# Kernel optimization log

Measured on AMD Instinct MI355X. Metric: run time of the kernel, lower is better.

## Reference

```python
import jax, jax.numpy as jnp
import numpy as np

DIM_MODEL = 1024
DIM_K = 1024
DIM_V = 1024


def setup_inputs() -> dict:
    key = jax.random.key(0)
    ks = jax.random.split(key, 7)
    B, S = 4, 2048
    scale = 1.0 / np.sqrt(DIM_MODEL)
    return {
        "x": jax.random.normal(ks[0], (B, S, DIM_MODEL), dtype=jnp.float32),
        # weights stored [in, out] (transpose of torch Linear.weight)
        "Wq": jax.random.normal(ks[1], (DIM_MODEL, DIM_K), dtype=jnp.float32) * scale,
        "Wk": jax.random.normal(ks[2], (DIM_MODEL, DIM_K), dtype=jnp.float32) * scale,
        "Wv": jax.random.normal(ks[3], (DIM_MODEL, DIM_V), dtype=jnp.float32) * scale,
        "Wo": jax.random.normal(ks[4], (DIM_V, DIM_MODEL), dtype=jnp.float32) * (1.0 / np.sqrt(DIM_V)),
        "ln2_gamma": jnp.ones((DIM_MODEL,), dtype=jnp.float32),
        "ln2_beta": jnp.zeros((DIM_MODEL,), dtype=jnp.float32),
    }


def _layernorm(x, gamma, beta, eps=1e-5):
    mu = jnp.mean(x, axis=-1, keepdims=True)
    var = jnp.var(x, axis=-1, keepdims=True)
    return (x - mu) * jax.lax.rsqrt(var + eps) * gamma + beta


def reference(x, Wq, Wk, Wv, Wo, ln2_gamma, ln2_beta):
    # single-head attention, x: [B,S,D]
    q = jnp.einsum("bsd,dk->bsk", x, Wq)
    k = jnp.einsum("bsd,dk->bsk", x, Wk)
    v = jnp.einsum("bsd,dv->bsv", x, Wv)
    scores = jnp.einsum("bqk,bsk->bqs", q, k) / jnp.sqrt(jnp.asarray(DIM_K, x.dtype))
    attn = jax.nn.softmax(scores, axis=-1)  # [B,S,S]
    ctx = jnp.einsum("bqs,bsv->bqv", attn, v)
    hidden = jnp.einsum("bqv,vd->bqd", ctx, Wo)
    hidden = _layernorm(hidden, ln2_gamma, ln2_beta)
    return hidden
```

## Files before the change

### kernel.cpp

```cpp
#include <hip/hip_runtime.h>
#include <hip/hip_bf16.h>
#include <stdint.h>

typedef __bf16 bf16;
typedef __attribute__((ext_vector_type(8))) __bf16 bf16x8;
typedef __attribute__((ext_vector_type(4))) __bf16 bf16x4;
typedef __attribute__((ext_vector_type(4))) float f32x4;

#define AS1 __attribute__((address_space(1)))
#define AS3 __attribute__((address_space(3)))

__device__ __forceinline__ void gl_lds16(const void* g, void* l) {
  __builtin_amdgcn_global_load_lds((const AS1 uint32_t*)g, (AS3 uint32_t*)l, 16, 0, 0);
}

#define FENCE() asm volatile("" ::: "memory")
#define BAR()                        \
  do {                               \
    FENCE();                         \
    __builtin_amdgcn_s_barrier();    \
    FENCE();                         \
  } while (0)
#define VMW4() asm volatile("s_waitcnt vmcnt(4)" ::: "memory")

template <int MODE>
__global__ __launch_bounds__(512, 2) void gemm256(
    const bf16* __restrict__ Abase, const bf16* __restrict__ Bbase,
    bf16* __restrict__ Cbase, int K, int lda, int ldb, int ldc,
    long long sA, long long sB, long long sC, float alpha,
    float* __restrict__ lsum, bf16* __restrict__ C2, bf16* __restrict__ C3) {
  extern __shared__ char smem[];
  const int z = blockIdx.z;
  const bf16* A = Abase + (long long)z * sA;
  const bf16* B = Bbase + (long long)z * sB;
  bf16* C = Cbase + (long long)z * sC;
  const int m0 = blockIdx.y * 256, n0 = blockIdx.x * 256;
  const int t = threadIdx.x;
  const int lane = t & 63;
  const int wid = t >> 6, wrow = wid >> 2, wcol = wid & 3;
  const int quad = lane >> 4, r = lane & 15;

  const int rowq = t >> 3;
  const int chunk = (t & 7) ^ (rowq & 7);
  const bf16* pA0 = A + (long long)(m0 + rowq) * lda + chunk * 8;
  const bf16* pB0 = B + (long long)(n0 + rowq) * ldb + chunk * 8;

  const int aoff = (wrow * 64 + r) * 128;
  const int boff = 32768 + (wcol * 32 + r) * 128;
  const int cs0 = ((quad) ^ (r & 7)) * 16;
  const int cs1 = ((4 + quad) ^ (r & 7)) * 16;

#define STAGE_A(HALF, KT, SB)                                                  \
  do {                                                                         \
    gl_lds16(pA0 + (long long)((HALF) * 128) * lda + (KT),                     \
             (SB) + (HALF) * 16384 + t * 16);                                  \
    gl_lds16(pA0 + (long long)((HALF) * 128 + 64) * lda + (KT),                \
             (SB) + (HALF) * 16384 + 8192 + t * 16);                           \
  } while (0)
#define STAGE_B(HALF, KT, SB)                                                  \
  do {                                                                         \
    gl_lds16(pB0 + (long long)((HALF) * 128) * ldb + (KT),                     \
             (SB) + 32768 + (HALF) * 16384 + t * 16);                          \
    gl_lds16(pB0 + (long long)((HALF) * 128 + 64) * ldb + (KT),                \
             (SB) + 32768 + (HALF) * 16384 + 8192 + t * 16);                   \
  } while (0)
#define READ_A(MH)                                                             \
  _Pragma("unroll") for (int mr = 0; mr < 4; ++mr) {                           \
    af[mr][0] = *(const bf16x8*)(Sc + (MH) * 16384 + aoff + mr * 2048 + cs0);  \
    af[mr][1] = *(const bf16x8*)(Sc + (MH) * 16384 + aoff + mr * 2048 + cs1);  \
  }
#define READ_B(NH)                                                             \
  _Pragma("unroll") for (int nr = 0; nr < 2; ++nr) {                           \
    bfr[NH][nr][0] =                                                           \
        *(const bf16x8*)(Sc + (NH) * 16384 + boff + nr * 2048 + cs0);          \
    bfr[NH][nr][1] =                                                           \
        *(const bf16x8*)(Sc + (NH) * 16384 + boff + nr * 2048 + cs1);          \
  }
#define MMA(MH, NH)                                                            \
  _Pragma("unroll") for (int mr = 0; mr < 4; ++mr)                             \
      _Pragma("unroll") for (int nr = 0; nr < 2; ++nr) {                       \
    acc[MH][NH][mr][nr] = __builtin_amdgcn_mfma_f32_16x16x32_bf16(             \
        af[mr][0], bfr[NH][nr][0], acc[MH][NH][mr][nr], 0, 0, 0);              \
    acc[MH][NH][mr][nr] = __builtin_amdgcn_mfma_f32_16x16x32_bf16(             \
        af[mr][1], bfr[NH][nr][1], acc[MH][NH][mr][nr], 0, 0, 0);              \
  }

  f32x4 acc[2][2][4][2] = {};
  bf16x8 af[4][2];
  bf16x8 bfr[2][2][2];
  char* Sc = smem;
  char* Sn = smem + 65536;
  const int T = K >> 6;

  STAGE_A(0, 0, Sc);
  STAGE_B(0, 0, Sc);
  STAGE_A(1, 0, Sc);
  STAGE_B(1, 0, Sc);
  {
    const int kt1p = (T > 1) ? 64 : 0;
    STAGE_A(0, kt1p, Sn);
    STAGE_B(0, kt1p, Sn);
  }
  VMW4();
  BAR();

  for (int tt = 0; tt < T; ++tt) {
    const int kt1 = (tt + 1 < T ? tt + 1 : 0) << 6;
    const int kt2 = (tt + 2 < T ? tt + 2 : 0) << 6;
    READ_A(0);
    READ_B(0);
    STAGE_A(1, kt1, Sn);
    __builtin_amdgcn_s_setprio(1);
    MMA(0, 0);
    __builtin_amdgcn_s_setprio(0);
    BAR();
    READ_B(1);
    STAGE_B(1, kt1, Sn);
    __builtin_amdgcn_s_setprio(1);
    MMA(0, 1);
    __builtin_amdgcn_s_setprio(0);
    BAR();
    READ_A(1);
    STAGE_A(0, kt2, Sc);
    __builtin_amdgcn_s_setprio(1);
    MMA(1, 0);
    __builtin_amdgcn_s_setprio(0);
    BAR();
    STAGE_B(0, kt2, Sc);
    __builtin_amdgcn_s_setprio(1);
    MMA(1, 1);
    __builtin_amdgcn_s_setprio(0);
    VMW4();
    BAR();
    char* tp = Sc;
    Sc = Sn;
    Sn = tp;
  }

  if constexpr (MODE == 4) {
    bf16* dst;
    int c0;
    if (n0 < 1024) {
      dst = Cbase;
      c0 = n0;
    } else if (n0 < 2048) {
      dst = C2;
      c0 = n0 - 1024;
    } else {
      dst = C3;
      c0 = n0 - 2048;
    }
#pragma unroll
    for (int mh = 0; mh < 2; ++mh)
#pragma unroll
      for (int mr = 0; mr < 4; ++mr) {
        const int row0 = m0 + mh * 128 + wrow * 64 + mr * 16 + quad * 4;
#pragma unroll
        for (int nh = 0; nh < 2; ++nh)
#pragma unroll
          for (int nr = 0; nr < 2; ++nr) {
            const int col = c0 + nh * 128 + wcol * 32 + nr * 16 + r;
#pragma unroll
            for (int rg = 0; rg < 4; ++rg)
              dst[(long long)(row0 + rg) * 1024 + col] =
                  (bf16)acc[mh][nh][mr][nr][rg];
          }
      }
    return;
  }

#pragma unroll
  for (int mh = 0; mh < 2; ++mh)
#pragma unroll
    for (int mr = 0; mr < 4; ++mr) {
      const int row0 = m0 + mh * 128 + wrow * 64 + mr * 16 + quad * 4;
      float rsum[4] = {0.f, 0.f, 0.f, 0.f};
#pragma unroll
      for (int nh = 0; nh < 2; ++nh)
#pragma unroll
        for (int nr = 0; nr < 2; ++nr) {
          const int col = n0 + nh * 128 + wcol * 32 + nr * 16 + r;
#pragma unroll
          for (int rg = 0; rg < 4; ++rg) {
            float v = acc[mh][nh][mr][nr][rg] * alpha;
            if constexpr (MODE == 1) {
              bf16 eb = (bf16)__expf(v);
              C[(long long)(row0 + rg) * ldc + col] = eb;
              rsum[rg] += (float)eb;
            } else {
              C[(long long)(row0 + rg) * ldc + col] = (bf16)v;
            }
          }
        }
      if constexpr (MODE == 1) {
#pragma unroll
        for (int rg = 0; rg < 4; ++rg) {
#pragma unroll
          for (int off = 8; off >= 1; off >>= 1)
            rsum[rg] += __shfl_xor(rsum[rg], off);
          if (r == 0)
            atomicAdd(&lsum[(long long)z * 2048 + row0 + rg], rsum[rg]);
        }
      }
    }
#undef STAGE_A
#undef STAGE_B
#undef READ_A
#undef READ_B
#undef MMA
}

template <int MODE>
__global__ __launch_bounds__(256, 3) void gemm128(
    const bf16* __restrict__ Abase, const bf16* __restrict__ Bbase,
    bf16* __restrict__ Cbase, int K, int lda, int ldb, int ldc,
    long long sA, long long sB, long long sC, float alpha,
    bf16* __restrict__ C2, bf16* __restrict__ C3) {
  extern __shared__ char smem[];
  const int z = blockIdx.z;
  const bf16* A = Abase + (long long)z * sA;
  const bf16* B = Bbase + (long long)z * sB;
  bf16* C = Cbase + (long long)z * sC;
  const int m0 = blockIdx.y * 128, n0 = blockIdx.x * 128;
  const int t = threadIdx.x;
  const int lane = t & 63, wave = t >> 6;
  const int wm = (wave >> 1) * 64, wn = (wave & 1) * 64;
  const int quad = lane >> 4, r = lane & 15;

  const int srow = t >> 3;
  const int schunk = (t & 7) ^ (srow & 7);
  const bf16* ga = A + (long long)(m0 + srow) * lda + schunk * 8;
  const bf16* gb = B + (long long)(n0 + srow) * ldb + schunk * 8;
  char* la = smem + t * 16;
  char* lb = smem + 16384 + t * 16;

  f32x4 acc[4][4] = {};

  for (int k0 = 0; k0 < K; k0 += 64) {
    __syncthreads();
#pragma unroll
    for (int rd = 0; rd < 4; rd++) {
      gl_lds16(ga + (long long)(32 * rd) * lda, la + rd * 4096);
      gl_lds16(gb + (long long)(32 * rd) * ldb, lb + rd * 4096);
    }
    ga += 64;
    gb += 64;
    __syncthreads();

#pragma unroll
    for (int kk = 0; kk < 2; kk++) {
      bf16x8 af[4], bfr[4];
      const int csa = ((kk * 4 + quad) ^ (r & 7)) * 16;
      const char* pa = smem + (wm + r) * 128 + csa;
      const char* pb = smem + 16384 + (wn + r) * 128 + csa;
#pragma unroll
      for (int i = 0; i < 4; i++) af[i] = *(const bf16x8*)(pa + i * 2048);
#pragma unroll
      for (int j = 0; j < 4; j++) bfr[j] = *(const bf16x8*)(pb + j * 2048);
#pragma unroll
      for (int i = 0; i < 4; i++)
#pragma unroll
        for (int j = 0; j < 4; j++)
          acc[i][j] = __builtin_amdgcn_mfma_f32_16x16x32_bf16(af[i], bfr[j],
                                                              acc[i][j], 0, 0, 0);
    }
  }

  if constexpr (MODE == 4) {
    bf16* dst;
    int c0;
    if (n0 < 1024) {
      dst = Cbase; c0 = n0;
    } else if (n0 < 2048) {
      dst = C2; c0 = n0 - 1024;
    } else {
      dst = C3; c0 = n0 - 2048;
    }
#pragma unroll
    for (int i = 0; i < 4; i++) {
      const int row0 = m0 + wm + i * 16 + quad * 4;
#pragma unroll
      for (int j = 0; j < 4; j++) {
        const int col = c0 + wn + j * 16 + r;
#pragma unroll
        for (int rg = 0; rg < 4; rg++)
          dst[(long long)(row0 + rg) * 1024 + col] = (bf16)acc[i][j][rg];
      }
    }
    return;
  }

#pragma unroll
  for (int i = 0; i < 4; i++) {
    const int row0 = m0 + wm + i * 16 + quad * 4;
#pragma unroll
    for (int j = 0; j < 4; j++) {
      const int col = n0 + wn + j * 16 + r;
#pragma unroll
      for (int rg = 0; rg < 4; rg++) {
        float v = acc[i][j][rg] * alpha;
        C[(long long)(row0 + rg) * ldc + col] = (bf16)v;
      }
    }
  }
}

__global__ __launch_bounds__(256) void prep(
    const float* __restrict__ x, const float* __restrict__ Wq,
    const float* __restrict__ Wk, const float* __restrict__ Wv,
    const float* __restrict__ Wo, bf16* __restrict__ Xb,
    bf16* __restrict__ Wcat, bf16* __restrict__ Wot,
    float* __restrict__ lsum) {
  __shared__ float tile[32][33];
  const int bx = blockIdx.x;
  const int t = threadIdx.x;
  if (bx < 4096) {
    if (bx < 32) lsum[bx * 256 + t] = 0.f;
    long long i = (long long)bx * 256 + t;
    const float4* p = (const float4*)x;
    float4 a = p[i * 2], b = p[i * 2 + 1];
    bf16x8 o;
    o[0] = (bf16)a.x; o[1] = (bf16)a.y; o[2] = (bf16)a.z; o[3] = (bf16)a.w;
    o[4] = (bf16)b.x; o[5] = (bf16)b.y; o[6] = (bf16)b.z; o[7] = (bf16)b.w;
    ((bf16x8*)Xb)[i] = o;
  } else {
    int idx = bx - 4096;
    const int zw = idx >> 10;
    idx &= 1023;
    const int tiy = idx >> 5, tix = idx & 31;
    const float* W = (zw == 0) ? Wq : (zw == 1) ? Wk : (zw == 2) ? Wv : Wo;
    bf16* dst = (zw < 3) ? (Wcat + (long long)zw * 1024 * 1024) : Wot;
    const int bx0 = tix * 32, by0 = tiy * 32;
    const int ttx = t & 31, tty = t >> 5;
#pragma unroll
    for (int i = 0; i < 32; i += 8)
      tile[tty + i][ttx] = W[(long long)(by0 + tty + i) * 1024 + bx0 + ttx];
    __syncthreads();
#pragma unroll
    for (int i = 0; i < 32; i += 8)
      dst[(long long)(bx0 + tty + i) * 1024 + by0 + ttx] = (bf16)tile[ttx][tty + i];
  }
}

__global__ __launch_bounds__(256) void layernorm_rows(
    const bf16* __restrict__ H, const float* __restrict__ lsum,
    const float* __restrict__ gamma, const float* __restrict__ beta,
    float* __restrict__ O) {
  const long long row = blockIdx.x;
  const bf16* h = H + row * 1024;
  float* o = O + row * 1024;
  const int t = threadIdx.x;
  const int lane = t & 63, wave = t >> 6;
  const float invl = 1.f / lsum[row];
  bf16x4 hv = ((const bf16x4*)h)[t];
  float v[4] = {(float)hv[0] * invl, (float)hv[1] * invl, (float)hv[2] * invl,
                (float)hv[3] * invl};
  float s = v[0] + v[1] + v[2] + v[3];
  float ss = v[0] * v[0] + v[1] * v[1] + v[2] * v[2] + v[3] * v[3];
#pragma unroll
  for (int off = 32; off >= 1; off >>= 1) {
    s += __shfl_xor(s, off);
    ss += __shfl_xor(ss, off);
  }
  __shared__ float rs[4], rss[4];
  if (lane == 0) {
    rs[wave] = s;
    rss[wave] = ss;
  }
  __syncthreads();
  s = rs[0] + rs[1] + rs[2] + rs[3];
  ss = rss[0] + rss[1] + rss[2] + rss[3];
  const float mean = s * (1.f / 1024.f);
  const float var = ss * (1.f / 1024.f) - mean * mean;
  const float rstd = rsqrtf(var + 1e-5f);
  float4 g = ((const float4*)gamma)[t];
  float4 bb = ((const float4*)beta)[t];
  float4 rr;
  rr.x = (v[0] - mean) * rstd * g.x + bb.x;
  rr.y = (v[1] - mean) * rstd * g.y + bb.y;
  rr.z = (v[2] - mean) * rstd * g.z + bb.z;
  rr.w = (v[3] - mean) * rstd * g.w + bb.w;
  ((float4*)o)[t] = rr;
}

extern "C" void kernel_launch(void* const* d_in, const int* in_sizes, int n_in,
                              void* d_out, int out_size, void* d_ws,
                              size_t ws_size, hipStream_t stream) {
  const float* x = (const float*)d_in[0];
  const float* Wq = (const float*)d_in[1];
  const float* Wk = (const float*)d_in[2];
  const float* Wv = (const float*)d_in[3];
  const float* Wo = (const float*)d_in[4];
  const float* gamma = (const float*)d_in[5];
  const float* beta = (const float*)d_in[6];
  float* out = (float*)d_out;

  char* ws = (char*)d_ws;
  const size_t MB = 1024ull * 1024ull;
  bf16* Xb = (bf16*)(ws + 0);
  bf16* Wcat = (bf16*)(ws + 16 * MB);
  bf16* Wot = (bf16*)(ws + 22 * MB);
  bf16* Qd = (bf16*)(ws + 24 * MB);
  bf16* Kd = (bf16*)(ws + 40 * MB);
  bf16* Vd = (bf16*)(ws + 56 * MB);
  bf16* expS = (bf16*)(ws + 72 * MB);
  float* lsum = (float*)(ws + 104 * MB);
  bf16* VWo = (bf16*)(ws + 105 * MB);
  bf16* Hd = (bf16*)(ws + 121 * MB);

  static hipStream_t s2 = nullptr;
  static hipEvent_t evA = nullptr, evB = nullptr;
  if (!s2) {
    hipStreamCreateWithFlags(&s2, hipStreamNonBlocking);
    hipEventCreateWithFlags(&evA, hipEventDisableTiming);
    hipEventCreateWithFlags(&evB, hipEventDisableTiming);
    hipFuncSetAttribute(reinterpret_cast<const void*>(&gemm256<1>),
                        hipFuncAttributeMaxDynamicSharedMemorySize, 131072);
  }

  prep<<<8192, 256, 0, stream>>>(x, Wq, Wk, Wv, Wo, Xb, Wcat, Wot, lsum);

  gemm128<4><<<dim3(24, 64, 1), 256, 32768, stream>>>(
      Xb, Wcat, Qd, 1024, 1024, 1024, 1024, 0, 0, 0, 1.f, Kd, Vd);

  hipEventRecord(evA, stream);
  hipStreamWaitEvent(s2, evA, 0);

  gemm128<0><<<dim3(16, 8, 4), 256, 32768, s2>>>(
      Wot, Vd, VWo, 1024, 1024, 1024, 2048, 0, 2048 * 1024LL, 1024 * 2048LL,
      1.f, nullptr, nullptr);
  hipEventRecord(evB, s2);

  gemm256<1><<<dim3(8, 8, 4), 512, 131072, stream>>>(
      Qd, Kd, expS, 1024, 1024, 1024, 2048, 2048 * 1024LL, 2048 * 1024LL,
      2048 * 2048LL, 0.03125f, lsum, nullptr, nullptr);

  hipStreamWaitEvent(stream, evB, 0);

  gemm128<0><<<dim3(8, 16, 4), 256, 32768, stream>>>(
      expS, VWo, Hd, 2048, 2048, 2048, 1024, 2048 * 2048LL, 1024 * 2048LL,
      2048 * 1024LL, 1.f, nullptr, nullptr);

  layernorm_rows<<<8192, 256, 0, stream>>>(Hd, lsum, gamma, beta, out);
}
```

Before: 273.3 us.

## Pad attention matrices, swizzle final GEMM blocks, and serialize on one stream

Pads the leading dimension of expS and VWo from 2048 to 2112 elements, which should avoid power-of-two stride conflicts in cache and memory channels. Adds an optional block-index swizzle to gemm128 that spreads consecutive workgroups across eight groups, used for the expS·VWo GEMM. Drops the second stream and its events, so the VWo GEMM now runs after the scores GEMM on the main stream. It also removes the dead MODE 4 branch from gemm256 and moves Hd to reuse the Xb workspace region; the trade-off is losing the overlap between the two streams.

```diff
diff --git a/kernel.cpp b/kernel.cpp
--- a/kernel.cpp
+++ b/kernel.cpp
@@ -137,38 +137,6 @@
     Sn = tp;
   }
 
-  if constexpr (MODE == 4) {
-    bf16* dst;
-    int c0;
-    if (n0 < 1024) {
-      dst = Cbase;
-      c0 = n0;
-    } else if (n0 < 2048) {
-      dst = C2;
-      c0 = n0 - 1024;
-    } else {
-      dst = C3;
-      c0 = n0 - 2048;
-    }
-#pragma unroll
-    for (int mh = 0; mh < 2; ++mh)
-#pragma unroll
-      for (int mr = 0; mr < 4; ++mr) {
-        const int row0 = m0 + mh * 128 + wrow * 64 + mr * 16 + quad * 4;
-#pragma unroll
-        for (int nh = 0; nh < 2; ++nh)
-#pragma unroll
-          for (int nr = 0; nr < 2; ++nr) {
-            const int col = c0 + nh * 128 + wcol * 32 + nr * 16 + r;
-#pragma unroll
-            for (int rg = 0; rg < 4; ++rg)
-              dst[(long long)(row0 + rg) * 1024 + col] =
-                  (bf16)acc[mh][nh][mr][nr][rg];
-          }
-      }
-    return;
-  }
-
 #pragma unroll
   for (int mh = 0; mh < 2; ++mh)
 #pragma unroll
@@ -210,18 +178,28 @@
 #undef MMA
 }
 
-template <int MODE>
+template <int MODE, bool SWZ>
 __global__ __launch_bounds__(256, 3) void gemm128(
     const bf16* __restrict__ Abase, const bf16* __restrict__ Bbase,
     bf16* __restrict__ Cbase, int K, int lda, int ldb, int ldc,
     long long sA, long long sB, long long sC, float alpha,
     bf16* __restrict__ C2, bf16* __restrict__ C3) {
   extern __shared__ char smem[];
-  const int z = blockIdx.z;
+  int bx = blockIdx.x, by = blockIdx.y, bz = blockIdx.z;
+  if constexpr (SWZ) {
+    const int gx = gridDim.x, gy = gridDim.y;
+    int id = bx + gx * (by + gy * bz);
+    const int q = (gx * gy * (int)gridDim.z) >> 3;
+    id = (id & 7) * q + (id >> 3);
+    bx = id % gx;
+    by = (id / gx) % gy;
+    bz = id / (gx * gy);
+  }
+  const int z = bz;
   const bf16* A = Abase + (long long)z * sA;
   const bf16* B = Bbase + (long long)z * sB;
   bf16* C = Cbase + (long long)z * sC;
-  const int m0 = blockIdx.y * 128, n0 = blockIdx.x * 128;
+  const int m0 = by * 128, n0 = bx * 128;
   const int t = threadIdx.x;
   const int lane = t & 63, wave = t >> 6;
   const int wm = (wave >> 1) * 64, wn = (wave & 1) * 64;
@@ -395,50 +373,43 @@
   const float* beta = (const float*)d_in[6];
   float* out = (float*)d_out;
 
+  const int LDP = 2112;
+
   char* ws = (char*)d_ws;
   const size_t MB = 1024ull * 1024ull;
   bf16* Xb = (bf16*)(ws + 0);
+  bf16* Hd = (bf16*)(ws + 0);
   bf16* Wcat = (bf16*)(ws + 16 * MB);
   bf16* Wot = (bf16*)(ws + 22 * MB);
   bf16* Qd = (bf16*)(ws + 24 * MB);
   bf16* Kd = (bf16*)(ws + 40 * MB);
   bf16* Vd = (bf16*)(ws + 56 * MB);
   bf16* expS = (bf16*)(ws + 72 * MB);
-  float* lsum = (float*)(ws + 104 * MB);
-  bf16* VWo = (bf16*)(ws + 105 * MB);
-  bf16* Hd = (bf16*)(ws + 121 * MB);
-
-  static hipStream_t s2 = nullptr;
-  static hipEvent_t evA = nullptr, evB = nullptr;
-  if (!s2) {
-    hipStreamCreateWithFlags(&s2, hipStreamNonBlocking);
-    hipEventCreateWithFlags(&evA, hipEventDisableTiming);
-    hipEventCreateWithFlags(&evB, hipEventDisableTiming);
+  float* lsum = (float*)(ws + 105 * MB);
+  bf16* VWo = (bf16*)(ws + 106 * MB);
+
+  static int inited = 0;
+  if (!inited) {
     hipFuncSetAttribute(reinterpret_cast<const void*>(&gemm256<1>),
                         hipFuncAttributeMaxDynamicSharedMemorySize, 131072);
+    inited = 1;
   }
 
   prep<<<8192, 256, 0, stream>>>(x, Wq, Wk, Wv, Wo, Xb, Wcat, Wot, lsum);
 
-  gemm128<4><<<dim3(24, 64, 1), 256, 32768, stream>>>(
+  gemm128<4, false><<<dim3(24, 64, 1), 256, 32768, stream>>>(
       Xb, Wcat, Qd, 1024, 1024, 1024, 1024, 0, 0, 0, 1.f, Kd, Vd);
 
-  hipEventRecord(evA, stream);
-  hipStreamWaitEvent(s2, evA, 0);
-
-  gemm128<0><<<dim3(16, 8, 4), 256, 32768, s2>>>(
-      Wot, Vd, VWo, 1024, 1024, 1024, 2048, 0, 2048 * 1024LL, 1024 * 2048LL,
+  gemm256<1><<<dim3(8, 8, 4), 512, 131072, stream>>>(
+      Qd, Kd, expS, 1024, 1024, 1024, LDP, 2048 * 1024LL, 2048 * 1024LL,
+      2048LL * LDP, 0.03125f, lsum, nullptr, nullptr);
+
+  gemm128<0, false><<<dim3(16, 8, 4), 256, 32768, stream>>>(
+      Wot, Vd, VWo, 1024, 1024, 1024, LDP, 0, 2048 * 1024LL, 1024LL * LDP,
       1.f, nullptr, nullptr);
-  hipEventRecord(evB, s2);
-
-  gemm256<1><<<dim3(8, 8, 4), 512, 131072, stream>>>(
-      Qd, Kd, expS, 1024, 1024, 1024, 2048, 2048 * 1024LL, 2048 * 1024LL,
-      2048 * 2048LL, 0.03125f, lsum, nullptr, nullptr);
-
-  hipStreamWaitEvent(stream, evB, 0);
-
-  gemm128<0><<<dim3(8, 16, 4), 256, 32768, stream>>>(
-      expS, VWo, Hd, 2048, 2048, 2048, 1024, 2048 * 2048LL, 1024 * 2048LL,
+
+  gemm128<0, true><<<dim3(8, 16, 4), 256, 32768, stream>>>(
+      expS, VWo, Hd, 2048, LDP, LDP, 1024, 2048LL * LDP, 1024LL * LDP,
       2048 * 1024LL, 1.f, nullptr, nullptr);
 
   layernorm_rows<<<8192, 256, 0, stream>>>(Hd, lsum, gamma, beta, out);
```

Measured after the change: 274.2 us. About the same (+0.3%).
